# Kernel tuning notes

Hardware: AMD Instinct MI355X
Metric: run time of the kernel (lower is better)

## Reference

```python
import jax, jax.numpy as jnp
import numpy as np
from jax.ops import segment_sum, segment_max

N_ENT = 50000
N_REL = 200
E = 800000
D = 128      # entity_dim
R = 128      # relation_dim
H = 8        # num_heads
HD = D // H  # head_dim
SLOPE = 0.2  # LeakyReLU negative slope

def leaky(x):
    return jnp.where(x >= 0, x, SLOPE * x)

def setup_inputs() -> dict:
    key = jax.random.key(0)
    ks = jax.random.split(key, 8)
    h = jax.random.normal(ks[0], (N_ENT, D), dtype=jnp.float32)
    z = jax.random.normal(ks[1], (N_REL, R), dtype=jnp.float32)
    # weights stored (in_features, out_features); scaled ~ kaiming-ish
    Wc_w = jax.random.normal(ks[2], (D + R, D), dtype=jnp.float32) / np.sqrt(D + R)
    P_w = jax.random.normal(ks[3], (2 * D + R, D), dtype=jnp.float32) / np.sqrt(2 * D + R)
    y_w = jax.random.normal(ks[4], (D, H), dtype=jnp.float32) / np.sqrt(D)
    residual_weight = jnp.ones((1,), dtype=jnp.float32)
    edge_index = jax.random.randint(ks[5], (2, E), 0, N_ENT, dtype=jnp.int32)
    edge_type = jax.random.randint(ks[6], (E,), 0, N_REL, dtype=jnp.int32)
    return {"h": h, "z": z, "Wc_w": Wc_w, "P_w": P_w, "y_w": y_w,
            "residual_weight": residual_weight,
            "edge_index": edge_index, "edge_type": edge_type}

def reference(h, z, Wc_w, P_w, y_w, residual_weight, edge_index, edge_type):
    src, dst = edge_index[0], edge_index[1]
    n = h.shape[0]
    # per-destination degree and mean relation embedding z_bar_i
    deg = segment_sum(jnp.ones_like(dst, dtype=h.dtype), dst, num_segments=n)  # (N,)
    z_edge = z[edge_type]                                                      # (E,R)
    z_bar = segment_sum(z_edge, dst, num_segments=n) / jnp.maximum(deg, 1.0)[:, None]  # (N,R)
    # split P_hat over the concat [h_i || h_j || z_k]
    P1, P2, P3 = P_w[:D], P_w[D:2 * D], P_w[2 * D:]
    hP1 = h @ P1   # (N,D) dst part
    hP2 = h @ P2   # (N,D) src part
    zP3 = z @ P3   # (N_REL,D)
    pre_edge = hP1[dst] + hP2[src] + zP3[edge_type]      # (E,D)
    attn_e = leaky(pre_edge) @ y_w                        # (E,H)
    pre_self = hP1 + hP2 + z_bar @ P3                     # (N,D)  b_self=[h_i,h_i,z_bar]
    attn_s = leaky(pre_self) @ y_w                        # (N,H)
    # segment softmax over {self} U incoming edges, per head
    m_e = segment_max(attn_e, dst, num_segments=n)        # -inf for empty segments
    m = jnp.maximum(attn_s, m_e)                          # (N,H)
    e_e = jnp.exp(attn_e - m[dst])                        # (E,H)
    e_s = jnp.exp(attn_s - m)                             # (N,H)
    denom = segment_sum(e_e, dst, num_segments=n) + e_s   # (N,H)
    w_e = e_e / denom[dst]                                # (E,H)
    w_s = e_s / denom                                     # (N,H)
    # Wc over concats [h || z]
    Wc_h, Wc_z = Wc_w[:D], Wc_w[D:]
    hWc = h @ Wc_h                                        # (N,D)
    zWc = z @ Wc_z                                        # (N_REL,D)
    t_e = hWc[src] + zWc[edge_type]                       # (E,D)
    t_s = hWc + z_bar @ Wc_z                              # (N,D)
    # per-head weighted sum
    agg_e = segment_sum(w_e[:, :, None] * t_e.reshape(-1, H, HD), dst, num_segments=n)
    agg = agg_e + w_s[:, :, None] * t_s.reshape(-1, H, HD)  # (N,H,HD)
    h_new = leaky(agg.reshape(-1, D) + residual_weight * h)
    # nodes without incoming edges keep their original representation
    return jnp.where(deg[:, None] > 0, h_new, h)
```

## Files before the change

### kernel.cpp

```cpp
#include <hip/hip_runtime.h>

#define NE 50000
#define NR 200
#define EE 800000
#define DD 128
#define HH 8
#define SLOTS 64
#define SLOPE 0.2f

__device__ __forceinline__ float leaky(float x){ return x >= 0.f ? x : SLOPE*x; }

__device__ __forceinline__ float head_reduce(float4 pa, float4 pb, int hh){
  bool b0 = (hh & 1) != 0;
  bool b1 = (hh & 2) != 0;
  bool b2 = (hh & 4) != 0;
  float q0 = (b0 ? pa.y : pa.x) + __shfl_xor(b0 ? pa.x : pa.y, 1, 64);
  float q1 = (b0 ? pa.w : pa.z) + __shfl_xor(b0 ? pa.z : pa.w, 1, 64);
  float q2 = (b0 ? pb.y : pb.x) + __shfl_xor(b0 ? pb.x : pb.y, 1, 64);
  float q3 = (b0 ? pb.w : pb.z) + __shfl_xor(b0 ? pb.z : pb.w, 1, 64);
  float r0 = (b1 ? q1 : q0) + __shfl_xor(b1 ? q0 : q1, 2, 64);
  float r1 = (b1 ? q3 : q2) + __shfl_xor(b1 ? q2 : q3, 2, 64);
  float a  = (b2 ? r1 : r0) + __shfl_xor(b2 ? r0 : r1, 4, 64);
  a += __shfl_xor(a, 8, 64);
  a += __shfl_xor(a, 16, 64);
  a += __shfl_xor(a, 32, 64);
  return a;
}

__device__ __forceinline__ float edge_attn(float2 p1, float2 a, float2 b,
    float4 A, float4 B, float4 C, float4 Dv, int hh){
  float l0 = leaky(p1.x + a.x + b.x);
  float l1 = leaky(p1.y + a.y + b.y);
  float4 pa, pb;
  pa.x = l0*A.x + l1*C.x;  pa.y = l0*A.y + l1*C.y;
  pa.z = l0*A.z + l1*C.z;  pa.w = l0*A.w + l1*C.w;
  pb.x = l0*B.x + l1*Dv.x; pb.y = l0*B.y + l1*Dv.y;
  pb.z = l0*B.z + l1*Dv.z; pb.w = l0*B.w + l1*Dv.w;
  return head_reduce(pa, pb, hh);
}

__device__ __forceinline__ void sm_update(float attn, float tx, float ty,
    float& m_h, float& den, float& aggx, float& aggy){
  float nm = fmaxf(m_h, attn);
  float sc = __expf(m_h - nm);
  float w  = __expf(attn - nm);
  den = den*sc + w;
  m_h = nm;
  aggx = aggx*sc + w*tx;
  aggy = aggy*sc + w*ty;
}

__global__ void k_zero(int* __restrict__ cnt){
  int i = blockIdx.x*256 + threadIdx.x;
  if (i < NE) cnt[i] = 0;
}

__global__ void k_scatter(const int* __restrict__ edge_index,
                          const int* __restrict__ edge_type,
                          int* __restrict__ cnt, int* __restrict__ slot){
  int e = blockIdx.x*256 + threadIdx.x;
  if (e >= EE) return;
  int s = edge_index[e];
  int d = edge_index[EE + e];
  int t = edge_type[e];
  int pos = atomicAdd(&cnt[d], 1);
  if (pos < SLOTS) slot[d*SLOTS + pos] = s | (t << 16);
}

__global__ void k_zsmall(const float* __restrict__ z, const float* __restrict__ P_w,
                         const float* __restrict__ Wc_w, float* __restrict__ zPW){
  int r = blockIdx.x, c = threadIdx.x;
  float a1 = 0.f, a2 = 0.f;
  for (int d = 0; d < DD; d++){
    float zv = z[r*DD + d];
    a1 = fmaf(zv, P_w[(2*DD + d)*DD + c], a1);
    a2 = fmaf(zv, Wc_w[(DD + d)*DD + c], a2);
  }
  zPW[(size_t)r*(2*DD) + c]      = a1;
  zPW[(size_t)r*(2*DD) + DD + c] = a2;
}

__global__ __launch_bounds__(256) void k_hgemm(const float* __restrict__ h,
    const float* __restrict__ P_w, const float* __restrict__ Wc_w,
    float* __restrict__ hP1, float* __restrict__ hPW){
  __shared__ float hs[64][DD + 4];
  int tid = threadIdx.x;
  int row0 = blockIdx.x * 64;
  for (int f = tid; f < 64*DD/4; f += 256){
    int r = f >> 5, c4 = f & 31;
    int gr = row0 + r;
    float4 v = (gr < NE) ? ((const float4*)(h + (size_t)gr*DD))[c4]
                         : make_float4(0.f,0.f,0.f,0.f);
    hs[r][c4*4+0] = v.x; hs[r][c4*4+1] = v.y;
    hs[r][c4*4+2] = v.z; hs[r][c4*4+3] = v.w;
  }
  __syncthreads();
  int r0 = (tid >> 4) * 4, c0 = (tid & 15) * 8;
  #pragma unroll
  for (int mi = 0; mi < 3; mi++){
    const float* W = (mi == 0) ? P_w : (mi == 1) ? (P_w + DD*DD) : Wc_w;
    float acc[4][8];
    #pragma unroll
    for (int i = 0; i < 4; i++)
      #pragma unroll
      for (int j = 0; j < 8; j++) acc[i][j] = 0.f;
    for (int d4 = 0; d4 < DD/4; d4++){
      float avs[4][4];
      #pragma unroll
      for (int i = 0; i < 4; i++)
        *(float4*)&avs[i][0] = *(const float4*)&hs[r0+i][d4*4];
      #pragma unroll
      for (int dd = 0; dd < 4; dd++){
        int d = d4*4 + dd;
        float4 b0 = *(const float4*)(W + d*DD + c0);
        float4 b1 = *(const float4*)(W + d*DD + c0 + 4);
        float bv[8] = {b0.x,b0.y,b0.z,b0.w,b1.x,b1.y,b1.z,b1.w};
        #pragma unroll
        for (int i = 0; i < 4; i++)
          #pragma unroll
          for (int j = 0; j < 8; j++)
            acc[i][j] = fmaf(avs[i][dd], bv[j], acc[i][j]);
      }
    }
    #pragma unroll
    for (int i = 0; i < 4; i++){
      int gr = row0 + r0 + i;
      if (gr < NE){
        float* O = (mi == 0) ? (hP1 + (size_t)gr*DD + c0)
                 : (mi == 1) ? (hPW + (size_t)gr*(2*DD) + c0)
                             : (hPW + (size_t)gr*(2*DD) + DD + c0);
        *(float4*)(O)     = make_float4(acc[i][0],acc[i][1],acc[i][2],acc[i][3]);
        *(float4*)(O + 4) = make_float4(acc[i][4],acc[i][5],acc[i][6],acc[i][7]);
      }
    }
  }
}

__global__ __launch_bounds__(256) void k_node(
    const float* __restrict__ hP1, const float* __restrict__ hPW,
    const float* __restrict__ zPW, const float* __restrict__ h,
    const float* __restrict__ y_w, const float* __restrict__ rw_p,
    const int* __restrict__ cnt, const int* __restrict__ slot,
    float* __restrict__ out){
  int lane = threadIdx.x & 63;
  int n = blockIdx.x*4 + (threadIdx.x >> 6);
  if (n >= NE) return;
  int hh  = lane & 7;
  int sub = lane >> 3;
  int di  = hh*8 + sub;
  int d0  = di*2;
  int deg = cnt[n]; if (deg > SLOTS) deg = SLOTS;
  float2 hn = ((const float2*)(h + (size_t)n*DD))[di];
  if (deg == 0){ ((float2*)(out + (size_t)n*DD))[di] = hn; return; }
  float2 p1  = ((const float2*)(hP1 + (size_t)n*DD))[di];
  const float* rowN = hPW + (size_t)n*(2*DD);
  float2 p2n = *(const float2*)(rowN + d0);
  float2 wcn = *(const float2*)(rowN + DD + d0);
  const float4* y4 = (const float4*)(y_w + (size_t)d0*HH);
  float4 A = y4[0], B = y4[1], C = y4[2], Dv = y4[3];
  int my_slot = 0;
  if (lane < deg) my_slot = slot[(size_t)n*SLOTS + lane];
  float m_h = -1e30f, den = 0.f;
  float aggx = 0.f, aggy = 0.f;
  float sP3x = 0.f, sP3y = 0.f, sWcx = 0.f, sWcy = 0.f;
  int j = 0;
  for (; j + 4 <= deg; j += 4){
    float2 av[4], bv[4], cv[4], ev[4];
    #pragma unroll
    for (int k = 0; k < 4; k++){
      int v = __builtin_amdgcn_readlane(my_slot, j + k);
      const float* rp = hPW + (size_t)(v & 0xFFFF)*(2*DD);
      const float* zp = zPW + (size_t)((unsigned)v >> 16)*(2*DD);
      av[k] = *(const float2*)(rp + d0);
      cv[k] = *(const float2*)(rp + DD + d0);
      bv[k] = *(const float2*)(zp + d0);
      ev[k] = *(const float2*)(zp + DD + d0);
    }
    float at[4];
    #pragma unroll
    for (int k = 0; k < 4; k++){
      sP3x += bv[k].x; sP3y += bv[k].y;
      sWcx += ev[k].x; sWcy += ev[k].y;
      at[k] = edge_attn(p1, av[k], bv[k], A, B, C, Dv, hh);
    }
    #pragma unroll
    for (int k = 0; k < 4; k++)
      sm_update(at[k], cv[k].x + ev[k].x, cv[k].y + ev[k].y, m_h, den, aggx, aggy);
  }
  for (; j < deg; j++){
    int v = __builtin_amdgcn_readlane(my_slot, j);
    const float* rp = hPW + (size_t)(v & 0xFFFF)*(2*DD);
    const float* zp = zPW + (size_t)((unsigned)v >> 16)*(2*DD);
    float2 a2 = *(const float2*)(rp + d0);
    float2 c2 = *(const float2*)(rp + DD + d0);
    float2 b2 = *(const float2*)(zp + d0);
    float2 e2 = *(const float2*)(zp + DD + d0);
    sP3x += b2.x; sP3y += b2.y;
    sWcx += e2.x; sWcy += e2.y;
    float at = edge_attn(p1, a2, b2, A, B, C, Dv, hh);
    sm_update(at, c2.x + e2.x, c2.y + e2.y, m_h, den, aggx, aggy);
  }
  float invdeg = 1.f/(float)deg;
  float2 zb1 = make_float2(sP3x*invdeg, sP3y*invdeg);
  float attnS = edge_attn(p1, p2n, zb1, A, B, C, Dv, hh);
  float nm = fmaxf(m_h, attnS);
  float sc = __expf(m_h - nm);
  float w  = __expf(attnS - nm);
  den = den*sc + w;
  float tx = wcn.x + sWcx*invdeg, ty = wcn.y + sWcy*invdeg;
  aggx = aggx*sc + w*tx;
  aggy = aggy*sc + w*ty;
  float rw = rw_p[0];
  float inv_den = 1.f/den;
  float o0 = leaky(aggx*inv_den + rw*hn.x);
  float o1 = leaky(aggy*inv_den + rw*hn.y);
  ((float2*)(out + (size_t)n*DD))[di] = make_float2(o0, o1);
}

extern "C" void kernel_launch(void* const* d_in, const int* in_sizes, int n_in,
                              void* d_out, int out_size, void* d_ws, size_t ws_size,
                              hipStream_t stream){
  const float* h    = (const float*)d_in[0];
  const float* z    = (const float*)d_in[1];
  const float* Wc_w = (const float*)d_in[2];
  const float* P_w  = (const float*)d_in[3];
  const float* y_w  = (const float*)d_in[4];
  const float* rw   = (const float*)d_in[5];
  const int* edge_index = (const int*)d_in[6];
  const int* edge_type  = (const int*)d_in[7];
  float* out = (float*)d_out;

  char* ws = (char*)d_ws;
  float* hP1 = (float*)ws;  ws += (size_t)NE*DD*4;
  float* hPW = (float*)ws;  ws += (size_t)NE*2*DD*4;
  float* zPW = (float*)ws;  ws += (size_t)NR*2*DD*4;
  int*   cnt = (int*)ws;    ws += (size_t)NE*4;
  int*   slot= (int*)ws;    ws += (size_t)NE*SLOTS*4;

  hipLaunchKernelGGL(k_zero,    dim3((NE+255)/256), dim3(256), 0, stream, cnt);
  hipLaunchKernelGGL(k_scatter, dim3((EE+255)/256), dim3(256), 0, stream,
                     edge_index, edge_type, cnt, slot);
  hipLaunchKernelGGL(k_zsmall,  dim3(NR), dim3(DD), 0, stream, z, P_w, Wc_w, zPW);
  hipLaunchKernelGGL(k_hgemm,   dim3((NE+63)/64), dim3(256), 0, stream,
                     h, P_w, Wc_w, hP1, hPW);
  hipLaunchKernelGGL(k_node,    dim3((NE+3)/4), dim3(256), 0, stream,
                     hP1, hPW, zPW, h, y_w, rw, cnt, slot, out);
}
```

Measured before the change: 452.9 us.

## Interleave hP2/Wc and zP3/zWc rows, drop online-softmax max tracking, unroll 8

```diff
diff --git a/kernel.cpp b/kernel.cpp
--- a/kernel.cpp
+++ b/kernel.cpp
@@ -27,27 +27,16 @@
   return a;
 }
 
-__device__ __forceinline__ float edge_attn(float2 p1, float2 a, float2 b,
-    float4 A, float4 B, float4 C, float4 Dv, int hh){
-  float l0 = leaky(p1.x + a.x + b.x);
-  float l1 = leaky(p1.y + a.y + b.y);
+__device__ __forceinline__ float edge_attn(float2 p1, float ax, float ay,
+    float bx, float by, float4 A, float4 B, float4 C, float4 Dv, int hh){
+  float l0 = leaky(p1.x + ax + bx);
+  float l1 = leaky(p1.y + ay + by);
   float4 pa, pb;
   pa.x = l0*A.x + l1*C.x;  pa.y = l0*A.y + l1*C.y;
   pa.z = l0*A.z + l1*C.z;  pa.w = l0*A.w + l1*C.w;
   pb.x = l0*B.x + l1*Dv.x; pb.y = l0*B.y + l1*Dv.y;
   pb.z = l0*B.z + l1*Dv.z; pb.w = l0*B.w + l1*Dv.w;
   return head_reduce(pa, pb, hh);
-}
-
-__device__ __forceinline__ void sm_update(float attn, float tx, float ty,
-    float& m_h, float& den, float& aggx, float& aggy){
-  float nm = fmaxf(m_h, attn);
-  float sc = __expf(m_h - nm);
-  float w  = __expf(attn - nm);
-  den = den*sc + w;
-  m_h = nm;
-  aggx = aggx*sc + w*tx;
-  aggy = aggy*sc + w*ty;
 }
 
 __global__ void k_zero(int* __restrict__ cnt){
@@ -76,8 +65,9 @@
     a1 = fmaf(zv, P_w[(2*DD + d)*DD + c], a1);
     a2 = fmaf(zv, Wc_w[(DD + d)*DD + c], a2);
   }
-  zPW[(size_t)r*(2*DD) + c]      = a1;
-  zPW[(size_t)r*(2*DD) + DD + c] = a2;
+  int di = c >> 1, lo = c & 1;
+  zPW[(size_t)r*(2*DD) + di*4 + lo]     = a1;
+  zPW[(size_t)r*(2*DD) + di*4 + 2 + lo] = a2;
 }
 
 __global__ __launch_bounds__(256) void k_hgemm(const float* __restrict__ h,
@@ -96,9 +86,7 @@
   }
   __syncthreads();
   int r0 = (tid >> 4) * 4, c0 = (tid & 15) * 8;
-  #pragma unroll
-  for (int mi = 0; mi < 3; mi++){
-    const float* W = (mi == 0) ? P_w : (mi == 1) ? (P_w + DD*DD) : Wc_w;
+  {
     float acc[4][8];
     #pragma unroll
     for (int i = 0; i < 4; i++)
@@ -112,8 +100,8 @@
       #pragma unroll
       for (int dd = 0; dd < 4; dd++){
         int d = d4*4 + dd;
-        float4 b0 = *(const float4*)(W + d*DD + c0);
-        float4 b1 = *(const float4*)(W + d*DD + c0 + 4);
+        float4 b0 = *(const float4*)(P_w + d*DD + c0);
+        float4 b1 = *(const float4*)(P_w + d*DD + c0 + 4);
         float bv[8] = {b0.x,b0.y,b0.z,b0.w,b1.x,b1.y,b1.z,b1.w};
         #pragma unroll
         for (int i = 0; i < 4; i++)
@@ -126,11 +114,49 @@
     for (int i = 0; i < 4; i++){
       int gr = row0 + r0 + i;
       if (gr < NE){
-        float* O = (mi == 0) ? (hP1 + (size_t)gr*DD + c0)
-                 : (mi == 1) ? (hPW + (size_t)gr*(2*DD) + c0)
-                             : (hPW + (size_t)gr*(2*DD) + DD + c0);
-        *(float4*)(O)     = make_float4(acc[i][0],acc[i][1],acc[i][2],acc[i][3]);
-        *(float4*)(O + 4) = make_float4(acc[i][4],acc[i][5],acc[i][6],acc[i][7]);
+        *(float4*)(hP1 + (size_t)gr*DD + c0)     = make_float4(acc[i][0],acc[i][1],acc[i][2],acc[i][3]);
+        *(float4*)(hP1 + (size_t)gr*DD + c0 + 4) = make_float4(acc[i][4],acc[i][5],acc[i][6],acc[i][7]);
+      }
+    }
+  }
+  {
+    float accA[4][8], accB[4][8];
+    #pragma unroll
+    for (int i = 0; i < 4; i++)
+      #pragma unroll
+      for (int j = 0; j < 8; j++){ accA[i][j] = 0.f; accB[i][j] = 0.f; }
+    const float* W2 = P_w + DD*DD;
+    for (int d4 = 0; d4 < DD/4; d4++){
+      float avs[4][4];
+      #pragma unroll
+      for (int i = 0; i < 4; i++)
+        *(float4*)&avs[i][0] = *(const float4*)&hs[r0+i][d4*4];
+      #pragma unroll
+      for (int dd = 0; dd < 4; dd++){
+        int d = d4*4 + dd;
+        float4 a0 = *(const float4*)(W2 + d*DD + c0);
+        float4 a1 = *(const float4*)(W2 + d*DD + c0 + 4);
+        float4 w0 = *(const float4*)(Wc_w + d*DD + c0);
+        float4 w1 = *(const float4*)(Wc_w + d*DD + c0 + 4);
+        float avv[8] = {a0.x,a0.y,a0.z,a0.w,a1.x,a1.y,a1.z,a1.w};
+        float wvv[8] = {w0.x,w0.y,w0.z,w0.w,w1.x,w1.y,w1.z,w1.w};
+        #pragma unroll
+        for (int i = 0; i < 4; i++)
+          #pragma unroll
+          for (int j = 0; j < 8; j++){
+            accA[i][j] = fmaf(avs[i][dd], avv[j], accA[i][j]);
+            accB[i][j] = fmaf(avs[i][dd], wvv[j], accB[i][j]);
+          }
+      }
+    }
+    #pragma unroll
+    for (int i = 0; i < 4; i++){
+      int gr = row0 + r0 + i;
+      if (gr < NE){
+        float4* orow = (float4*)(hPW + (size_t)gr*(2*DD)) + (c0 >> 1);
+        #pragma unroll
+        for (int q = 0; q < 4; q++)
+          orow[q] = make_float4(accA[i][2*q], accA[i][2*q+1], accB[i][2*q], accB[i][2*q+1]);
       }
     }
   }
@@ -149,67 +175,53 @@
   int sub = lane >> 3;
   int di  = hh*8 + sub;
   int d0  = di*2;
-  int deg = cnt[n]; if (deg > SLOTS) deg = SLOTS;
+  int degv = cnt[n]; if (degv > SLOTS) degv = SLOTS;
+  int deg = __builtin_amdgcn_readfirstlane(degv);
   float2 hn = ((const float2*)(h + (size_t)n*DD))[di];
   if (deg == 0){ ((float2*)(out + (size_t)n*DD))[di] = hn; return; }
-  float2 p1  = ((const float2*)(hP1 + (size_t)n*DD))[di];
-  const float* rowN = hPW + (size_t)n*(2*DD);
-  float2 p2n = *(const float2*)(rowN + d0);
-  float2 wcn = *(const float2*)(rowN + DD + d0);
+  float2 p1 = ((const float2*)(hP1 + (size_t)n*DD))[di];
+  float4 pwn = ((const float4*)(hPW + (size_t)n*(2*DD)))[di];
   const float4* y4 = (const float4*)(y_w + (size_t)d0*HH);
   float4 A = y4[0], B = y4[1], C = y4[2], Dv = y4[3];
   int my_slot = 0;
   if (lane < deg) my_slot = slot[(size_t)n*SLOTS + lane];
-  float m_h = -1e30f, den = 0.f;
-  float aggx = 0.f, aggy = 0.f;
+  float den = 0.f, aggx = 0.f, aggy = 0.f;
   float sP3x = 0.f, sP3y = 0.f, sWcx = 0.f, sWcy = 0.f;
-  int j = 0;
-  for (; j + 4 <= deg; j += 4){
-    float2 av[4], bv[4], cv[4], ev[4];
-    #pragma unroll
-    for (int k = 0; k < 4; k++){
-      int v = __builtin_amdgcn_readlane(my_slot, j + k);
-      const float* rp = hPW + (size_t)(v & 0xFFFF)*(2*DD);
-      const float* zp = zPW + (size_t)((unsigned)v >> 16)*(2*DD);
-      av[k] = *(const float2*)(rp + d0);
-      cv[k] = *(const float2*)(rp + DD + d0);
-      bv[k] = *(const float2*)(zp + d0);
-      ev[k] = *(const float2*)(zp + DD + d0);
-    }
-    float at[4];
-    #pragma unroll
-    for (int k = 0; k < 4; k++){
-      sP3x += bv[k].x; sP3y += bv[k].y;
-      sWcx += ev[k].x; sWcy += ev[k].y;
-      at[k] = edge_attn(p1, av[k], bv[k], A, B, C, Dv, hh);
-    }
-    #pragma unroll
-    for (int k = 0; k < 4; k++)
-      sm_update(at[k], cv[k].x + ev[k].x, cv[k].y + ev[k].y, m_h, den, aggx, aggy);
-  }
-  for (; j < deg; j++){
-    int v = __builtin_amdgcn_readlane(my_slot, j);
-    const float* rp = hPW + (size_t)(v & 0xFFFF)*(2*DD);
-    const float* zp = zPW + (size_t)((unsigned)v >> 16)*(2*DD);
-    float2 a2 = *(const float2*)(rp + d0);
-    float2 c2 = *(const float2*)(rp + DD + d0);
-    float2 b2 = *(const float2*)(zp + d0);
-    float2 e2 = *(const float2*)(zp + DD + d0);
-    sP3x += b2.x; sP3y += b2.y;
-    sWcx += e2.x; sWcy += e2.y;
-    float at = edge_attn(p1, a2, b2, A, B, C, Dv, hh);
-    sm_update(at, c2.x + e2.x, c2.y + e2.y, m_h, den, aggx, aggy);
+  for (int j0 = 0; j0 < deg; j0 += 8){
+    float4 hv[8], zv[8];
+    #pragma unroll
+    for (int k = 0; k < 8; k++){
+      int jj = j0 + k;
+      int v = __builtin_amdgcn_readlane(my_slot, jj < SLOTS ? jj : 0);
+      const float4* rp = (const float4*)(hPW + (size_t)(v & 0xFFFF)*(2*DD));
+      const float4* zp = (const float4*)(zPW + (size_t)((unsigned)v >> 16)*(2*DD));
+      hv[k] = rp[di];
+      zv[k] = zp[di];
+    }
+    #pragma unroll
+    for (int k = 0; k < 8; k++){
+      if (j0 + k >= deg){ zv[k].x = 0.f; zv[k].y = 0.f; zv[k].z = 0.f; zv[k].w = 0.f; }
+      sP3x += zv[k].x; sP3y += zv[k].y;
+      sWcx += zv[k].z; sWcy += zv[k].w;
+    }
+    float at[8];
+    #pragma unroll
+    for (int k = 0; k < 8; k++)
+      at[k] = edge_attn(p1, hv[k].x, hv[k].y, zv[k].x, zv[k].y, A, B, C, Dv, hh);
+    #pragma unroll
+    for (int k = 0; k < 8; k++){
+      float w = (j0 + k < deg) ? __expf(at[k]) : 0.f;
+      den += w;
+      aggx = fmaf(w, hv[k].z + zv[k].z, aggx);
+      aggy = fmaf(w, hv[k].w + zv[k].w, aggy);
+    }
   }
   float invdeg = 1.f/(float)deg;
-  float2 zb1 = make_float2(sP3x*invdeg, sP3y*invdeg);
-  float attnS = edge_attn(p1, p2n, zb1, A, B, C, Dv, hh);
-  float nm = fmaxf(m_h, attnS);
-  float sc = __expf(m_h - nm);
-  float w  = __expf(attnS - nm);
-  den = den*sc + w;
-  float tx = wcn.x + sWcx*invdeg, ty = wcn.y + sWcy*invdeg;
-  aggx = aggx*sc + w*tx;
-  aggy = aggy*sc + w*ty;
+  float attnS = edge_attn(p1, pwn.x, pwn.y, sP3x*invdeg, sP3y*invdeg, A, B, C, Dv, hh);
+  float wS = __expf(attnS);
+  den += wS;
+  aggx = fmaf(wS, pwn.z + sWcx*invdeg, aggx);
+  aggy = fmaf(wS, pwn.w + sWcy*invdeg, aggy);
   float rw = rw_p[0];
   float inv_den = 1.f/den;
   float o0 = leaky(aggx*inv_den + rw*hn.x);
```

After: 562.4 us. 1.24x slower.
